# Optimization experiments

Measured on AMD Instinct MI355X. Metric: run time of the kernel, lower is better.

The kernel has to match this reference:

```python
import jax, jax.numpy as jnp
import numpy as np

N_NODES = 100000


def gcn_conv(x, W, b, src, dst, num_nodes):
    # PyG GCNConv: add self-loops, symmetric normalization, x @ W, scatter-add, + b
    xw = x @ W  # [N, out]
    loop = jnp.arange(num_nodes, dtype=src.dtype)
    s = jnp.concatenate([src, loop])  # message source j
    d = jnp.concatenate([dst, loop])  # aggregation target i
    deg = jax.ops.segment_sum(jnp.ones_like(d, dtype=xw.dtype), d, num_segments=num_nodes)
    dis = jnp.where(deg > 0, jax.lax.rsqrt(deg), 0.0)  # D^{-1/2}
    norm = dis[s] * dis[d]  # [E+N]
    msg = norm[:, None] * xw[s]  # gather + scale
    out = jax.ops.segment_sum(msg, d, num_segments=num_nodes)  # scatter-add
    return out + b


def setup_inputs() -> dict:
    key = jax.random.key(0)
    k1, k2, k3, k4 = jax.random.split(key, 4)
    F, H, E = 64, 64, 1250000
    x = jax.random.normal(k1, (N_NODES, F), dtype=jnp.float32)
    edge_index = jax.random.randint(k2, (2, E), 0, N_NODES, dtype=jnp.int64)
    W1 = jax.random.normal(k3, (F, H), dtype=jnp.float32) * (1.0 / np.sqrt(F))
    b1 = jnp.zeros((H,), dtype=jnp.float32)
    W2 = jax.random.normal(k4, (H, F), dtype=jnp.float32) * (1.0 / np.sqrt(H))
    b2 = jnp.zeros((F,), dtype=jnp.float32)
    return {"x": x, "edge_index": edge_index, "W1": W1, "b1": b1, "W2": W2, "b2": b2}


def reference(x, edge_index, W1, b1, W2, b2):
    src, dst = edge_index[0], edge_index[1]
    h = gcn_conv(x, W1, b1, src, dst, N_NODES)
    h = jax.nn.relu(h)
    out = gcn_conv(h, W2, b2, src, dst, N_NODES)
    return out
```

## Files before the change

kernel.cpp:

```cpp
#include <hip/hip_runtime.h>

#define NN    100000
#define F     64
#define NBUCK 391
#define CAPB  4096
#define TILE  4096
#define G1A   1600
#define G1TOT 3125

#define O_CURSOR 0
#define O_ROWPTR 512
#define O_DEG    100864
#define O_DIS    201216
#define O_PACKED 301568
#define O_SRT    1903104
#define O_AH     3504768
#define O_BH     6704768

__device__ __forceinline__ unsigned bf_rne(float x) {
    unsigned u = __float_as_uint(x);
    return (u + 0x7FFFu + ((u >> 16) & 1u)) >> 16;
}
__device__ __forceinline__ unsigned pack2(float lo, float hi) {
    return bf_rne(lo) | (bf_rne(hi) << 16);
}
__device__ __forceinline__ float lo_f(unsigned u) { return __uint_as_float(u << 16); }
__device__ __forceinline__ float hi_f(unsigned u) { return __uint_as_float(u & 0xFFFF0000u); }

struct BpSmem {
    int hist[NBUCK], lofs[NBUCK], gbase[NBUCK], lcur[NBUCK];
    int wsum[8];
    unsigned stage[TILE];
    unsigned short sbuck[TILE];
};
union KSmem {
    BpSmem bp;
    float wl[64 * 64];
};
struct NsSmem {
    int h[256], lcur[256], wsum[4];
    int stage[CAPB];
};
union K2Smem {
    NsSmem ns;
    float wl[64 * 64];
};

__device__ __forceinline__ void binpack_body(const int* __restrict__ src,
                                             const int* __restrict__ dst, int E,
                                             int* __restrict__ cursor,
                                             unsigned* __restrict__ packed,
                                             int bid, BpSmem& sm) {
    int t  = threadIdx.x;
    int t0 = bid * TILE;
    int n  = min(TILE, E - t0);

    if (t < NBUCK) sm.hist[t] = 0;
    __syncthreads();
    for (int i = t; i < n; i += 512) atomicAdd(&sm.hist[dst[t0 + i] >> 8], 1);
    __syncthreads();
    int lane = t & 63, w = t >> 6;
    int v = (t < NBUCK) ? sm.hist[t] : 0;
    int s = v;
#pragma unroll
    for (int off = 1; off < 64; off <<= 1) {
        int u = __shfl_up(s, off, 64);
        if (lane >= off) s += u;
    }
    if (lane == 63) sm.wsum[w] = s;
    __syncthreads();
    if (t == 0) {
        int run = 0;
#pragma unroll
        for (int i = 0; i < 8; ++i) { int c = sm.wsum[i]; sm.wsum[i] = run; run += c; }
    }
    __syncthreads();
    if (t < NBUCK) {
        int ex = s - v + sm.wsum[w];
        sm.lofs[t] = ex;
        sm.lcur[t] = ex;
        sm.gbase[t] = t * CAPB + (v ? atomicAdd(&cursor[t], v) : 0);
    }
    __syncthreads();
    for (int i = t; i < n; i += 512) {
        int d = dst[t0 + i];
        int b = d >> 8;
        int p = atomicAdd(&sm.lcur[b], 1);
        sm.stage[p] = ((unsigned)src[t0 + i] << 8) | (unsigned)(d & 255);
        sm.sbuck[p] = (unsigned short)b;
    }
    __syncthreads();
    for (int i = t; i < n; i += 512) {
        int b = sm.sbuck[i];
        packed[sm.gbase[b] + (i - sm.lofs[b])] = sm.stage[i];
    }
}

__device__ __forceinline__ void gemm_body(const float* __restrict__ X,
                                          const float* __restrict__ W,
                                          unsigned* __restrict__ Ah, int bid,
                                          float* wl) {
    int t = threadIdx.x;
    for (int i = t; i < 64 * 64; i += 512) wl[i] = W[i];
    __syncthreads();
    int lane = t & 63;
    int w    = t >> 6;
    float Wreg[64];
#pragma unroll
    for (int k = 0; k < 64; ++k) Wreg[k] = wl[k * 64 + lane];

    int row0 = bid * 32 + w * 4;
    const float* xp = X + (size_t)row0 * F;
    float xa = xp[lane];
    float xb = xp[64 + lane];
    float xc = xp[128 + lane];
    float xd = xp[192 + lane];
    float a0 = 0.f, a1 = 0.f, a2 = 0.f, a3 = 0.f;
#pragma unroll
    for (int k = 0; k < 64; ++k) {
        float wv = Wreg[k];
        a0 = fmaf(__uint_as_float(__builtin_amdgcn_readlane(__float_as_uint(xa), k)), wv, a0);
        a1 = fmaf(__uint_as_float(__builtin_amdgcn_readlane(__float_as_uint(xb), k)), wv, a1);
        a2 = fmaf(__uint_as_float(__builtin_amdgcn_readlane(__float_as_uint(xc), k)), wv, a2);
        a3 = fmaf(__uint_as_float(__builtin_amdgcn_readlane(__float_as_uint(xd), k)), wv, a3);
    }
    float p0 = __shfl_xor(a0, 1, 64);
    float p1 = __shfl_xor(a1, 1, 64);
    float p2 = __shfl_xor(a2, 1, 64);
    float p3 = __shfl_xor(a3, 1, 64);
    if (!(lane & 1)) {
        int c = lane >> 1;
        Ah[(size_t)(row0 + 0) * 32 + c] = pack2(a0, p0);
        Ah[(size_t)(row0 + 1) * 32 + c] = pack2(a1, p1);
        Ah[(size_t)(row0 + 2) * 32 + c] = pack2(a2, p2);
        Ah[(size_t)(row0 + 3) * 32 + c] = pack2(a3, p3);
    }
}

__device__ __forceinline__ void node_sort_body(const unsigned* __restrict__ packed,
                                               const int* __restrict__ cursor,
                                               int* __restrict__ row_ptr,
                                               int* __restrict__ deg,
                                               float* __restrict__ dis,
                                               int* __restrict__ srt,
                                               int b, NsSmem& sm) {
    int t = threadIdx.x;
    int nbase = b << 8;
    int nloc = min(256, NN - nbase);
    int beg = b * CAPB;
    int n = cursor[b];

    if (t < 256) sm.h[t] = 0;
    __syncthreads();
    for (int i = t; i < n; i += 512)
        atomicAdd(&sm.h[packed[beg + i] & 255u], 1);
    __syncthreads();
    int lane = t & 63, w = t >> 6;
    int v = 0, s = 0;
    if (t < 256) { v = sm.h[t]; s = v; }
#pragma unroll
    for (int off = 1; off < 64; off <<= 1) {
        int u = __shfl_up(s, off, 64);
        if (lane >= off) s += u;
    }
    if (t < 256 && lane == 63) sm.wsum[w] = s;
    __syncthreads();
    if (t == 0) {
        int run = 0;
#pragma unroll
        for (int i = 0; i < 4; ++i) { int c = sm.wsum[i]; sm.wsum[i] = run; run += c; }
    }
    __syncthreads();
    if (t < 256) {
        int e0 = s - v + sm.wsum[w];
        sm.lcur[t] = e0;
        if (t < nloc) {
            row_ptr[nbase + t] = beg + e0;
            deg[nbase + t]     = v;
            dis[nbase + t]     = rsqrtf((float)v + 1.0f);
        }
    }
    __syncthreads();
    for (int i = t; i < n; i += 512) {
        unsigned p = packed[beg + i];
        int pos = atomicAdd(&sm.lcur[p & 255u], 1);
        sm.stage[pos] = (int)(p >> 8);
    }
    __syncthreads();
    for (int i = t; i < n; i += 512) srt[beg + i] = sm.stage[i];
}

__global__ __launch_bounds__(512) void pre_gemm1(const int* __restrict__ src,
                                                 const int* __restrict__ dst, int E,
                                                 int nbp, int* __restrict__ cursor,
                                                 unsigned* __restrict__ packed,
                                                 const float* __restrict__ X,
                                                 const float* __restrict__ W1,
                                                 unsigned* __restrict__ Ah) {
    __shared__ KSmem sm;
    if ((int)blockIdx.x < nbp)
        binpack_body(src, dst, E, cursor, packed, blockIdx.x, sm.bp);
    else
        gemm_body(X, W1, Ah, (int)blockIdx.x - nbp, sm.wl);
}

__global__ __launch_bounds__(512) void sort_gemm1(const unsigned* __restrict__ packed,
                                                  const int* __restrict__ cursor,
                                                  int* __restrict__ row_ptr,
                                                  int* __restrict__ deg,
                                                  float* __restrict__ dis,
                                                  int* __restrict__ srt,
                                                  const float* __restrict__ X,
                                                  const float* __restrict__ W1,
                                                  unsigned* __restrict__ Ah) {
    __shared__ K2Smem sm;
    if ((int)blockIdx.x < NBUCK)
        node_sort_body(packed, cursor, row_ptr, deg, dis, srt, blockIdx.x, sm.ns);
    else
        gemm_body(X, W1, Ah, G1A + (int)blockIdx.x - NBUCK, sm.wl);
}

__global__ __launch_bounds__(256) void agg1_gemm2(const uint2* __restrict__ Ah2,
                                                  const int* __restrict__ row_ptr,
                                                  const int* __restrict__ deg,
                                                  const int* __restrict__ srt,
                                                  const float* __restrict__ dis,
                                                  const float* __restrict__ b1,
                                                  const float* __restrict__ W2,
                                                  unsigned* __restrict__ Bh) {
    __shared__ float wl[64 * 64];
    int t = threadIdx.x;
    for (int i = t; i < 64 * 64; i += 256) wl[i] = W2[i];
    __syncthreads();

    int sub  = t & 15;
    int node = blockIdx.x * 16 + (t >> 4);
    int beg = row_ptr[node];
    int end = beg + deg[node];
    float di = dis[node];
    uint2 su = Ah2[(size_t)node * 16 + sub];
    float4 acc;
    acc.x = di * lo_f(su.x);
    acc.y = di * hi_f(su.x);
    acc.z = di * lo_f(su.y);
    acc.w = di * hi_f(su.y);
    int j = beg;
    for (; j + 4 <= end; j += 4) {
        int s0 = srt[j], s1 = srt[j + 1], s2 = srt[j + 2], s3 = srt[j + 3];
        float d0 = dis[s0], d1 = dis[s1], d2 = dis[s2], d3 = dis[s3];
        uint2 g0 = Ah2[(size_t)s0 * 16 + sub];
        uint2 g1 = Ah2[(size_t)s1 * 16 + sub];
        uint2 g2 = Ah2[(size_t)s2 * 16 + sub];
        uint2 g3 = Ah2[(size_t)s3 * 16 + sub];
        acc.x = fmaf(d0, lo_f(g0.x), fmaf(d1, lo_f(g1.x), fmaf(d2, lo_f(g2.x), fmaf(d3, lo_f(g3.x), acc.x))));
        acc.y = fmaf(d0, hi_f(g0.x), fmaf(d1, hi_f(g1.x), fmaf(d2, hi_f(g2.x), fmaf(d3, hi_f(g3.x), acc.y))));
        acc.z = fmaf(d0, lo_f(g0.y), fmaf(d1, lo_f(g1.y), fmaf(d2, lo_f(g2.y), fmaf(d3, lo_f(g3.y), acc.z))));
        acc.w = fmaf(d0, hi_f(g0.y), fmaf(d1, hi_f(g1.y), fmaf(d2, hi_f(g2.y), fmaf(d3, hi_f(g3.y), acc.w))));
    }
    for (; j < end; ++j) {
        int s0 = srt[j];
        float d0 = dis[s0];
        uint2 g0 = Ah2[(size_t)s0 * 16 + sub];
        acc.x = fmaf(d0, lo_f(g0.x), acc.x);
        acc.y = fmaf(d0, hi_f(g0.x), acc.y);
        acc.z = fmaf(d0, lo_f(g0.y), acc.z);
        acc.w = fmaf(d0, hi_f(g0.y), acc.w);
    }
    float4 bb = ((const float4*)b1)[sub];
    float4 o;
    o.x = fmaxf(fmaf(di, acc.x, bb.x), 0.f);
    o.y = fmaxf(fmaf(di, acc.y, bb.y), 0.f);
    o.z = fmaxf(fmaf(di, acc.z, bb.z), 0.f);
    o.w = fmaxf(fmaf(di, acc.w, bb.w), 0.f);
    unsigned pkx = pack2(o.x, o.y);
    unsigned pky = pack2(o.z, o.w);

    int lane = t & 63;
    float a0 = 0.f, a1 = 0.f, a2 = 0.f, a3 = 0.f;
#pragma unroll
    for (int kq = 0; kq < 16; ++kq) {
        float w0 = wl[(4 * kq + 0) * 64 + lane];
        float w1 = wl[(4 * kq + 1) * 64 + lane];
        float w2 = wl[(4 * kq + 2) * 64 + lane];
        float w3 = wl[(4 * kq + 3) * 64 + lane];
        unsigned qx0 = __builtin_amdgcn_readlane(pkx, kq);
        unsigned qy0 = __builtin_amdgcn_readlane(pky, kq);
        unsigned qx1 = __builtin_amdgcn_readlane(pkx, 16 + kq);
        unsigned qy1 = __builtin_amdgcn_readlane(pky, 16 + kq);
        unsigned qx2 = __builtin_amdgcn_readlane(pkx, 32 + kq);
        unsigned qy2 = __builtin_amdgcn_readlane(pky, 32 + kq);
        unsigned qx3 = __builtin_amdgcn_readlane(pkx, 48 + kq);
        unsigned qy3 = __builtin_amdgcn_readlane(pky, 48 + kq);
        a0 = fmaf(lo_f(qx0), w0, a0); a0 = fmaf(hi_f(qx0), w1, a0);
        a0 = fmaf(lo_f(qy0), w2, a0); a0 = fmaf(hi_f(qy0), w3, a0);
        a1 = fmaf(lo_f(qx1), w0, a1); a1 = fmaf(hi_f(qx1), w1, a1);
        a1 = fmaf(lo_f(qy1), w2, a1); a1 = fmaf(hi_f(qy1), w3, a1);
        a2 = fmaf(lo_f(qx2), w0, a2); a2 = fmaf(hi_f(qx2), w1, a2);
        a2 = fmaf(lo_f(qy2), w2, a2); a2 = fmaf(hi_f(qy2), w3, a2);
        a3 = fmaf(lo_f(qx3), w0, a3); a3 = fmaf(hi_f(qx3), w1, a3);
        a3 = fmaf(lo_f(qy3), w2, a3); a3 = fmaf(hi_f(qy3), w3, a3);
    }
    float p0 = __shfl_xor(a0, 1, 64);
    float p1 = __shfl_xor(a1, 1, 64);
    float p2 = __shfl_xor(a2, 1, 64);
    float p3 = __shfl_xor(a3, 1, 64);
    if (!(lane & 1)) {
        int c = lane >> 1;
        int row0 = blockIdx.x * 16 + (t >> 6) * 4;
        Bh[(size_t)(row0 + 0) * 32 + c] = pack2(a0, p0);
        Bh[(size_t)(row0 + 1) * 32 + c] = pack2(a1, p1);
        Bh[(size_t)(row0 + 2) * 32 + c] = pack2(a2, p2);
        Bh[(size_t)(row0 + 3) * 32 + c] = pack2(a3, p3);
    }
}

__global__ __launch_bounds__(256) void agg_out(const uint2* __restrict__ Ah2,
                                               const int* __restrict__ row_ptr,
                                               const int* __restrict__ deg,
                                               const int* __restrict__ srt,
                                               const float* __restrict__ dis,
                                               const float* __restrict__ bias,
                                               float* __restrict__ outp) {
    int sub  = threadIdx.x & 15;
    int node = blockIdx.x * 16 + (threadIdx.x >> 4);
    int beg = row_ptr[node];
    int end = beg + deg[node];
    float di = dis[node];
    uint2 su = Ah2[(size_t)node * 16 + sub];
    float4 acc;
    acc.x = di * lo_f(su.x);
    acc.y = di * hi_f(su.x);
    acc.z = di * lo_f(su.y);
    acc.w = di * hi_f(su.y);
    int j = beg;
    for (; j + 4 <= end; j += 4) {
        int s0 = srt[j], s1 = srt[j + 1], s2 = srt[j + 2], s3 = srt[j + 3];
        float d0 = dis[s0], d1 = dis[s1], d2 = dis[s2], d3 = dis[s3];
        uint2 g0 = Ah2[(size_t)s0 * 16 + sub];
        uint2 g1 = Ah2[(size_t)s1 * 16 + sub];
        uint2 g2 = Ah2[(size_t)s2 * 16 + sub];
        uint2 g3 = Ah2[(size_t)s3 * 16 + sub];
        acc.x = fmaf(d0, lo_f(g0.x), fmaf(d1, lo_f(g1.x), fmaf(d2, lo_f(g2.x), fmaf(d3, lo_f(g3.x), acc.x))));
        acc.y = fmaf(d0, hi_f(g0.x), fmaf(d1, hi_f(g1.x), fmaf(d2, hi_f(g2.x), fmaf(d3, hi_f(g3.x), acc.y))));
        acc.z = fmaf(d0, lo_f(g0.y), fmaf(d1, lo_f(g1.y), fmaf(d2, lo_f(g2.y), fmaf(d3, lo_f(g3.y), acc.z))));
        acc.w = fmaf(d0, hi_f(g0.y), fmaf(d1, hi_f(g1.y), fmaf(d2, hi_f(g2.y), fmaf(d3, hi_f(g3.y), acc.w))));
    }
    for (; j < end; ++j) {
        int s0 = srt[j];
        float d0 = dis[s0];
        uint2 g0 = Ah2[(size_t)s0 * 16 + sub];
        acc.x = fmaf(d0, lo_f(g0.x), acc.x);
        acc.y = fmaf(d0, hi_f(g0.x), acc.y);
        acc.z = fmaf(d0, lo_f(g0.y), acc.z);
        acc.w = fmaf(d0, hi_f(g0.y), acc.w);
    }
    float4 bb = ((const float4*)bias)[sub];
    float4 o;
    o.x = fmaf(di, acc.x, bb.x);
    o.y = fmaf(di, acc.y, bb.y);
    o.z = fmaf(di, acc.z, bb.z);
    o.w = fmaf(di, acc.w, bb.w);
    ((float4*)outp)[(size_t)node * 16 + sub] = o;
}

extern "C" void kernel_launch(void* const* d_in, const int* in_sizes, int n_in,
                              void* d_out, int out_size, void* d_ws, size_t ws_size,
                              hipStream_t stream) {
    const float* x  = (const float*)d_in[0];
    const int*   ei = (const int*)d_in[1];
    const float* W1 = (const float*)d_in[2];
    const float* b1 = (const float*)d_in[3];
    const float* W2 = (const float*)d_in[4];
    const float* b2 = (const float*)d_in[5];
    float* out = (float*)d_out;
    int E = in_sizes[1] / 2;
    const int* src = ei;
    const int* dst = ei + E;

    int*      ws_i    = (int*)d_ws;
    int*      cursor  = ws_i + O_CURSOR;
    int*      row_ptr = ws_i + O_ROWPTR;
    int*      deg     = ws_i + O_DEG;
    float*    dis     = (float*)(ws_i + O_DIS);
    unsigned* packed  = (unsigned*)(ws_i + O_PACKED);
    int*      srt     = ws_i + O_SRT;
    unsigned* Ah      = (unsigned*)(ws_i + O_AH);
    unsigned* Bh      = (unsigned*)(ws_i + O_BH);

    int nbp = (E + TILE - 1) / TILE;

    hipMemsetAsync(cursor, 0, NBUCK * sizeof(int), stream);
    pre_gemm1<<<nbp + G1A, 512, 0, stream>>>(src, dst, E, nbp, cursor, packed,
                                             x, W1, Ah);
    sort_gemm1<<<NBUCK + (G1TOT - G1A), 512, 0, stream>>>(packed, cursor, row_ptr,
                                                          deg, dis, srt, x, W1, Ah);
    agg1_gemm2<<<NN / 16, 256, 0, stream>>>((const uint2*)Ah, row_ptr, deg, srt,
                                            dis, b1, W2, Bh);
    agg_out<<<NN / 16, 256, 0, stream>>>((const uint2*)Bh, row_ptr, deg, srt,
                                         dis, b2, out);
}
```

Baseline: 200.7 us.

## Use 16-byte gathers with two-way edge split and prescale layer-2 output by dis

The two aggregation kernels now have each lane gather a uint4 (8 bf16 features) instead of a uint2. The 16 threads per node are split into two groups that take alternating edges and combine their partial sums with a cross-lane shuffle. The layer-2 GEMM output is premultiplied by the source node's dis, so the final aggregation drops the per-edge dis lookup and multiply. This aims to cut memory transactions and per-edge dependent loads, but adds a reduction shuffle and uses more registers per thread.

```diff
diff --git a/kernel.cpp b/kernel.cpp
--- a/kernel.cpp
+++ b/kernel.cpp
@@ -220,7 +220,7 @@
         gemm_body(X, W1, Ah, G1A + (int)blockIdx.x - NBUCK, sm.wl);
 }
 
-__global__ __launch_bounds__(256) void agg1_gemm2(const uint2* __restrict__ Ah2,
+__global__ __launch_bounds__(256) void agg1_gemm2(const uint4* __restrict__ Ah4,
                                                   const int* __restrict__ row_ptr,
                                                   const int* __restrict__ deg,
                                                   const int* __restrict__ srt,
@@ -230,137 +230,219 @@
                                                   unsigned* __restrict__ Bh) {
     __shared__ float wl[64 * 64];
     int t = threadIdx.x;
-    for (int i = t; i < 64 * 64; i += 256) wl[i] = W2[i];
-    __syncthreads();
-
-    int sub  = t & 15;
+    for (int i = t; i < 1024; i += 256)
+        ((float4*)wl)[i] = ((const float4*)W2)[i];
+    __syncthreads();
+
+    int sub  = t & 7;
+    int grp  = (t >> 3) & 1;
     int node = blockIdx.x * 16 + (t >> 4);
     int beg = row_ptr[node];
     int end = beg + deg[node];
     float di = dis[node];
-    uint2 su = Ah2[(size_t)node * 16 + sub];
-    float4 acc;
-    acc.x = di * lo_f(su.x);
-    acc.y = di * hi_f(su.x);
-    acc.z = di * lo_f(su.y);
-    acc.w = di * hi_f(su.y);
-    int j = beg;
-    for (; j + 4 <= end; j += 4) {
-        int s0 = srt[j], s1 = srt[j + 1], s2 = srt[j + 2], s3 = srt[j + 3];
+
+    float a0, a1, a2, a3, a4, a5, a6, a7;
+    uint4 su = Ah4[(size_t)node * 8 + sub];
+    if (grp == 0) {
+        a0 = di * lo_f(su.x); a1 = di * hi_f(su.x);
+        a2 = di * lo_f(su.y); a3 = di * hi_f(su.y);
+        a4 = di * lo_f(su.z); a5 = di * hi_f(su.z);
+        a6 = di * lo_f(su.w); a7 = di * hi_f(su.w);
+    } else {
+        a0 = a1 = a2 = a3 = a4 = a5 = a6 = a7 = 0.f;
+    }
+
+    int j = beg + grp;
+    for (; j + 6 < end; j += 8) {
+        int s0 = srt[j], s1 = srt[j + 2], s2 = srt[j + 4], s3 = srt[j + 6];
         float d0 = dis[s0], d1 = dis[s1], d2 = dis[s2], d3 = dis[s3];
-        uint2 g0 = Ah2[(size_t)s0 * 16 + sub];
-        uint2 g1 = Ah2[(size_t)s1 * 16 + sub];
-        uint2 g2 = Ah2[(size_t)s2 * 16 + sub];
-        uint2 g3 = Ah2[(size_t)s3 * 16 + sub];
-        acc.x = fmaf(d0, lo_f(g0.x), fmaf(d1, lo_f(g1.x), fmaf(d2, lo_f(g2.x), fmaf(d3, lo_f(g3.x), acc.x))));
-        acc.y = fmaf(d0, hi_f(g0.x), fmaf(d1, hi_f(g1.x), fmaf(d2, hi_f(g2.x), fmaf(d3, hi_f(g3.x), acc.y))));
-        acc.z = fmaf(d0, lo_f(g0.y), fmaf(d1, lo_f(g1.y), fmaf(d2, lo_f(g2.y), fmaf(d3, lo_f(g3.y), acc.z))));
-        acc.w = fmaf(d0, hi_f(g0.y), fmaf(d1, hi_f(g1.y), fmaf(d2, hi_f(g2.y), fmaf(d3, hi_f(g3.y), acc.w))));
-    }
-    for (; j < end; ++j) {
+        uint4 g0 = Ah4[(size_t)s0 * 8 + sub];
+        uint4 g1 = Ah4[(size_t)s1 * 8 + sub];
+        uint4 g2 = Ah4[(size_t)s2 * 8 + sub];
+        uint4 g3 = Ah4[(size_t)s3 * 8 + sub];
+        a0 = fmaf(d0, lo_f(g0.x), fmaf(d1, lo_f(g1.x), fmaf(d2, lo_f(g2.x), fmaf(d3, lo_f(g3.x), a0))));
+        a1 = fmaf(d0, hi_f(g0.x), fmaf(d1, hi_f(g1.x), fmaf(d2, hi_f(g2.x), fmaf(d3, hi_f(g3.x), a1))));
+        a2 = fmaf(d0, lo_f(g0.y), fmaf(d1, lo_f(g1.y), fmaf(d2, lo_f(g2.y), fmaf(d3, lo_f(g3.y), a2))));
+        a3 = fmaf(d0, hi_f(g0.y), fmaf(d1, hi_f(g1.y), fmaf(d2, hi_f(g2.y), fmaf(d3, hi_f(g3.y), a3))));
+        a4 = fmaf(d0, lo_f(g0.z), fmaf(d1, lo_f(g1.z), fmaf(d2, lo_f(g2.z), fmaf(d3, lo_f(g3.z), a4))));
+        a5 = fmaf(d0, hi_f(g0.z), fmaf(d1, hi_f(g1.z), fmaf(d2, hi_f(g2.z), fmaf(d3, hi_f(g3.z), a5))));
+        a6 = fmaf(d0, lo_f(g0.w), fmaf(d1, lo_f(g1.w), fmaf(d2, lo_f(g2.w), fmaf(d3, lo_f(g3.w), a6))));
+        a7 = fmaf(d0, hi_f(g0.w), fmaf(d1, hi_f(g1.w), fmaf(d2, hi_f(g2.w), fmaf(d3, hi_f(g3.w), a7))));
+    }
+    for (; j + 2 < end; j += 4) {
+        int s0 = srt[j], s1 = srt[j + 2];
+        float d0 = dis[s0], d1 = dis[s1];
+        uint4 g0 = Ah4[(size_t)s0 * 8 + sub];
+        uint4 g1 = Ah4[(size_t)s1 * 8 + sub];
+        a0 = fmaf(d0, lo_f(g0.x), fmaf(d1, lo_f(g1.x), a0));
+        a1 = fmaf(d0, hi_f(g0.x), fmaf(d1, hi_f(g1.x), a1));
+        a2 = fmaf(d0, lo_f(g0.y), fmaf(d1, lo_f(g1.y), a2));
+        a3 = fmaf(d0, hi_f(g0.y), fmaf(d1, hi_f(g1.y), a3));
+        a4 = fmaf(d0, lo_f(g0.z), fmaf(d1, lo_f(g1.z), a4));
+        a5 = fmaf(d0, hi_f(g0.z), fmaf(d1, hi_f(g1.z), a5));
+        a6 = fmaf(d0, lo_f(g0.w), fmaf(d1, lo_f(g1.w), a6));
+        a7 = fmaf(d0, hi_f(g0.w), fmaf(d1, hi_f(g1.w), a7));
+    }
+    for (; j < end; j += 2) {
         int s0 = srt[j];
         float d0 = dis[s0];
-        uint2 g0 = Ah2[(size_t)s0 * 16 + sub];
-        acc.x = fmaf(d0, lo_f(g0.x), acc.x);
-        acc.y = fmaf(d0, hi_f(g0.x), acc.y);
-        acc.z = fmaf(d0, lo_f(g0.y), acc.z);
-        acc.w = fmaf(d0, hi_f(g0.y), acc.w);
-    }
-    float4 bb = ((const float4*)b1)[sub];
-    float4 o;
-    o.x = fmaxf(fmaf(di, acc.x, bb.x), 0.f);
-    o.y = fmaxf(fmaf(di, acc.y, bb.y), 0.f);
-    o.z = fmaxf(fmaf(di, acc.z, bb.z), 0.f);
-    o.w = fmaxf(fmaf(di, acc.w, bb.w), 0.f);
-    unsigned pkx = pack2(o.x, o.y);
-    unsigned pky = pack2(o.z, o.w);
+        uint4 g0 = Ah4[(size_t)s0 * 8 + sub];
+        a0 = fmaf(d0, lo_f(g0.x), a0);
+        a1 = fmaf(d0, hi_f(g0.x), a1);
+        a2 = fmaf(d0, lo_f(g0.y), a2);
+        a3 = fmaf(d0, hi_f(g0.y), a3);
+        a4 = fmaf(d0, lo_f(g0.z), a4);
+        a5 = fmaf(d0, hi_f(g0.z), a5);
+        a6 = fmaf(d0, lo_f(g0.w), a6);
+        a7 = fmaf(d0, hi_f(g0.w), a7);
+    }
+    a0 += __shfl_xor(a0, 8, 64); a1 += __shfl_xor(a1, 8, 64);
+    a2 += __shfl_xor(a2, 8, 64); a3 += __shfl_xor(a3, 8, 64);
+    a4 += __shfl_xor(a4, 8, 64); a5 += __shfl_xor(a5, 8, 64);
+    a6 += __shfl_xor(a6, 8, 64); a7 += __shfl_xor(a7, 8, 64);
+
+    float4 bb0 = ((const float4*)b1)[2 * sub];
+    float4 bb1 = ((const float4*)b1)[2 * sub + 1];
+    float o0 = fmaxf(fmaf(di, a0, bb0.x), 0.f);
+    float o1 = fmaxf(fmaf(di, a1, bb0.y), 0.f);
+    float o2 = fmaxf(fmaf(di, a2, bb0.z), 0.f);
+    float o3 = fmaxf(fmaf(di, a3, bb0.w), 0.f);
+    float o4 = fmaxf(fmaf(di, a4, bb1.x), 0.f);
+    float o5 = fmaxf(fmaf(di, a5, bb1.y), 0.f);
+    float o6 = fmaxf(fmaf(di, a6, bb1.z), 0.f);
+    float o7 = fmaxf(fmaf(di, a7, bb1.w), 0.f);
+    unsigned pk0 = pack2(o0, o1);
+    unsigned pk1 = pack2(o2, o3);
+    unsigned pk2 = pack2(o4, o5);
+    unsigned pk3 = pack2(o6, o7);
 
     int lane = t & 63;
-    float a0 = 0.f, a1 = 0.f, a2 = 0.f, a3 = 0.f;
-#pragma unroll
-    for (int kq = 0; kq < 16; ++kq) {
-        float w0 = wl[(4 * kq + 0) * 64 + lane];
-        float w1 = wl[(4 * kq + 1) * 64 + lane];
-        float w2 = wl[(4 * kq + 2) * 64 + lane];
-        float w3 = wl[(4 * kq + 3) * 64 + lane];
-        unsigned qx0 = __builtin_amdgcn_readlane(pkx, kq);
-        unsigned qy0 = __builtin_amdgcn_readlane(pky, kq);
-        unsigned qx1 = __builtin_amdgcn_readlane(pkx, 16 + kq);
-        unsigned qy1 = __builtin_amdgcn_readlane(pky, 16 + kq);
-        unsigned qx2 = __builtin_amdgcn_readlane(pkx, 32 + kq);
-        unsigned qy2 = __builtin_amdgcn_readlane(pky, 32 + kq);
-        unsigned qx3 = __builtin_amdgcn_readlane(pkx, 48 + kq);
-        unsigned qy3 = __builtin_amdgcn_readlane(pky, 48 + kq);
-        a0 = fmaf(lo_f(qx0), w0, a0); a0 = fmaf(hi_f(qx0), w1, a0);
-        a0 = fmaf(lo_f(qy0), w2, a0); a0 = fmaf(hi_f(qy0), w3, a0);
-        a1 = fmaf(lo_f(qx1), w0, a1); a1 = fmaf(hi_f(qx1), w1, a1);
-        a1 = fmaf(lo_f(qy1), w2, a1); a1 = fmaf(hi_f(qy1), w3, a1);
-        a2 = fmaf(lo_f(qx2), w0, a2); a2 = fmaf(hi_f(qx2), w1, a2);
-        a2 = fmaf(lo_f(qy2), w2, a2); a2 = fmaf(hi_f(qy2), w3, a2);
-        a3 = fmaf(lo_f(qx3), w0, a3); a3 = fmaf(hi_f(qx3), w1, a3);
-        a3 = fmaf(lo_f(qy3), w2, a3); a3 = fmaf(hi_f(qy3), w3, a3);
-    }
-    float p0 = __shfl_xor(a0, 1, 64);
-    float p1 = __shfl_xor(a1, 1, 64);
-    float p2 = __shfl_xor(a2, 1, 64);
-    float p3 = __shfl_xor(a3, 1, 64);
+    float c0 = 0.f, c1 = 0.f, c2 = 0.f, c3 = 0.f;
+#pragma unroll
+    for (int l8 = 0; l8 < 8; ++l8) {
+#define STEP(PK, P)                                                        \
+        {                                                                  \
+            int k0 = l8 * 8 + 2 * (P);                                     \
+            float w0 = wl[k0 * 64 + lane];                                 \
+            float w1 = wl[k0 * 64 + 64 + lane];                            \
+            unsigned u0 = __builtin_amdgcn_readlane(PK, l8);               \
+            unsigned u1 = __builtin_amdgcn_readlane(PK, 16 + l8);          \
+            unsigned u2 = __builtin_amdgcn_readlane(PK, 32 + l8);          \
+            unsigned u3 = __builtin_amdgcn_readlane(PK, 48 + l8);          \
+            c0 = fmaf(lo_f(u0), w0, c0); c0 = fmaf(hi_f(u0), w1, c0);      \
+            c1 = fmaf(lo_f(u1), w0, c1); c1 = fmaf(hi_f(u1), w1, c1);      \
+            c2 = fmaf(lo_f(u2), w0, c2); c2 = fmaf(hi_f(u2), w1, c2);      \
+            c3 = fmaf(lo_f(u3), w0, c3); c3 = fmaf(hi_f(u3), w1, c3);      \
+        }
+        STEP(pk0, 0)
+        STEP(pk1, 1)
+        STEP(pk2, 2)
+        STEP(pk3, 3)
+#undef STEP
+    }
+    float dA = __shfl(di, 0, 64);
+    float dB = __shfl(di, 16, 64);
+    float dC = __shfl(di, 32, 64);
+    float dD = __shfl(di, 48, 64);
+    c0 *= dA; c1 *= dB; c2 *= dC; c3 *= dD;
+    float q0 = __shfl_xor(c0, 1, 64);
+    float q1 = __shfl_xor(c1, 1, 64);
+    float q2 = __shfl_xor(c2, 1, 64);
+    float q3 = __shfl_xor(c3, 1, 64);
     if (!(lane & 1)) {
         int c = lane >> 1;
-        int row0 = blockIdx.x * 16 + (t >> 6) * 4;
-        Bh[(size_t)(row0 + 0) * 32 + c] = pack2(a0, p0);
-        Bh[(size_t)(row0 + 1) * 32 + c] = pack2(a1, p1);
-        Bh[(size_t)(row0 + 2) * 32 + c] = pack2(a2, p2);
-        Bh[(size_t)(row0 + 3) * 32 + c] = pack2(a3, p3);
-    }
-}
-
-__global__ __launch_bounds__(256) void agg_out(const uint2* __restrict__ Ah2,
+        int n0 = blockIdx.x * 16 + (t >> 6) * 4;
+        Bh[(size_t)(n0 + 0) * 32 + c] = pack2(c0, q0);
+        Bh[(size_t)(n0 + 1) * 32 + c] = pack2(c1, q1);
+        Bh[(size_t)(n0 + 2) * 32 + c] = pack2(c2, q2);
+        Bh[(size_t)(n0 + 3) * 32 + c] = pack2(c3, q3);
+    }
+}
+
+__global__ __launch_bounds__(256) void agg_out(const uint4* __restrict__ Bs4,
                                                const int* __restrict__ row_ptr,
                                                const int* __restrict__ deg,
                                                const int* __restrict__ srt,
                                                const float* __restrict__ dis,
                                                const float* __restrict__ bias,
                                                float* __restrict__ outp) {
-    int sub  = threadIdx.x & 15;
-    int node = blockIdx.x * 16 + (threadIdx.x >> 4);
+    int t = threadIdx.x;
+    int sub  = t & 7;
+    int grp  = (t >> 3) & 1;
+    int node = blockIdx.x * 16 + (t >> 4);
     int beg = row_ptr[node];
     int end = beg + deg[node];
     float di = dis[node];
-    uint2 su = Ah2[(size_t)node * 16 + sub];
-    float4 acc;
-    acc.x = di * lo_f(su.x);
-    acc.y = di * hi_f(su.x);
-    acc.z = di * lo_f(su.y);
-    acc.w = di * hi_f(su.y);
-    int j = beg;
-    for (; j + 4 <= end; j += 4) {
-        int s0 = srt[j], s1 = srt[j + 1], s2 = srt[j + 2], s3 = srt[j + 3];
-        float d0 = dis[s0], d1 = dis[s1], d2 = dis[s2], d3 = dis[s3];
-        uint2 g0 = Ah2[(size_t)s0 * 16 + sub];
-        uint2 g1 = Ah2[(size_t)s1 * 16 + sub];
-        uint2 g2 = Ah2[(size_t)s2 * 16 + sub];
-        uint2 g3 = Ah2[(size_t)s3 * 16 + sub];
-        acc.x = fmaf(d0, lo_f(g0.x), fmaf(d1, lo_f(g1.x), fmaf(d2, lo_f(g2.x), fmaf(d3, lo_f(g3.x), acc.x))));
-        acc.y = fmaf(d0, hi_f(g0.x), fmaf(d1, hi_f(g1.x), fmaf(d2, hi_f(g2.x), fmaf(d3, hi_f(g3.x), acc.y))));
-        acc.z = fmaf(d0, lo_f(g0.y), fmaf(d1, lo_f(g1.y), fmaf(d2, lo_f(g2.y), fmaf(d3, lo_f(g3.y), acc.z))));
-        acc.w = fmaf(d0, hi_f(g0.y), fmaf(d1, hi_f(g1.y), fmaf(d2, hi_f(g2.y), fmaf(d3, hi_f(g3.y), acc.w))));
-    }
-    for (; j < end; ++j) {
+
+    float a0, a1, a2, a3, a4, a5, a6, a7;
+    uint4 su = Bs4[(size_t)node * 8 + sub];
+    if (grp == 0) {
+        a0 = lo_f(su.x); a1 = hi_f(su.x);
+        a2 = lo_f(su.y); a3 = hi_f(su.y);
+        a4 = lo_f(su.z); a5 = hi_f(su.z);
+        a6 = lo_f(su.w); a7 = hi_f(su.w);
+    } else {
+        a0 = a1 = a2 = a3 = a4 = a5 = a6 = a7 = 0.f;
+    }
+
+    int j = beg + grp;
+    for (; j + 6 < end; j += 8) {
+        int s0 = srt[j], s1 = srt[j + 2], s2 = srt[j + 4], s3 = srt[j + 6];
+        uint4 g0 = Bs4[(size_t)s0 * 8 + sub];
+        uint4 g1 = Bs4[(size_t)s1 * 8 + sub];
+        uint4 g2 = Bs4[(size_t)s2 * 8 + sub];
+        uint4 g3 = Bs4[(size_t)s3 * 8 + sub];
+        a0 += (lo_f(g0.x) + lo_f(g1.x)) + (lo_f(g2.x) + lo_f(g3.x));
+        a1 += (hi_f(g0.x) + hi_f(g1.x)) + (hi_f(g2.x) + hi_f(g3.x));
+        a2 += (lo_f(g0.y) + lo_f(g1.y)) + (lo_f(g2.y) + lo_f(g3.y));
+        a3 += (hi_f(g0.y) + hi_f(g1.y)) + (hi_f(g2.y) + hi_f(g3.y));
+        a4 += (lo_f(g0.z) + lo_f(g1.z)) + (lo_f(g2.z) + lo_f(g3.z));
+        a5 += (hi_f(g0.z) + hi_f(g1.z)) + (hi_f(g2.z) + hi_f(g3.z));
+        a6 += (lo_f(g0.w) + lo_f(g1.w)) + (lo_f(g2.w) + lo_f(g3.w));
+        a7 += (hi_f(g0.w) + hi_f(g1.w)) + (hi_f(g2.w) + hi_f(g3.w));
+    }
+    for (; j + 2 < end; j += 4) {
+        int s0 = srt[j], s1 = srt[j + 2];
+        uint4 g0 = Bs4[(size_t)s0 * 8 + sub];
+        uint4 g1 = Bs4[(size_t)s1 * 8 + sub];
+        a0 += lo_f(g0.x) + lo_f(g1.x);
+        a1 += hi_f(g0.x) + hi_f(g1.x);
+        a2 += lo_f(g0.y) + lo_f(g1.y);
+        a3 += hi_f(g0.y) + hi_f(g1.y);
+        a4 += lo_f(g0.z) + lo_f(g1.z);
+        a5 += hi_f(g0.z) + hi_f(g1.z);
+        a6 += lo_f(g0.w) + lo_f(g1.w);
+        a7 += hi_f(g0.w) + hi_f(g1.w);
+    }
+    for (; j < end; j += 2) {
         int s0 = srt[j];
-        float d0 = dis[s0];
-        uint2 g0 = Ah2[(size_t)s0 * 16 + sub];
-        acc.x = fmaf(d0, lo_f(g0.x), acc.x);
-        acc.y = fmaf(d0, hi_f(g0.x), acc.y);
-        acc.z = fmaf(d0, lo_f(g0.y), acc.z);
-        acc.w = fmaf(d0, hi_f(g0.y), acc.w);
-    }
-    float4 bb = ((const float4*)bias)[sub];
+        uint4 g0 = Bs4[(size_t)s0 * 8 + sub];
+        a0 += lo_f(g0.x); a1 += hi_f(g0.x);
+        a2 += lo_f(g0.y); a3 += hi_f(g0.y);
+        a4 += lo_f(g0.z); a5 += hi_f(g0.z);
+        a6 += lo_f(g0.w); a7 += hi_f(g0.w);
+    }
+    a0 += __shfl_xor(a0, 8, 64); a1 += __shfl_xor(a1, 8, 64);
+    a2 += __shfl_xor(a2, 8, 64); a3 += __shfl_xor(a3, 8, 64);
+    a4 += __shfl_xor(a4, 8, 64); a5 += __shfl_xor(a5, 8, 64);
+    a6 += __shfl_xor(a6, 8, 64); a7 += __shfl_xor(a7, 8, 64);
+
+    float4 bb0 = ((const float4*)bias)[2 * sub];
+    float4 bb1 = ((const float4*)bias)[2 * sub + 1];
     float4 o;
-    o.x = fmaf(di, acc.x, bb.x);
-    o.y = fmaf(di, acc.y, bb.y);
-    o.z = fmaf(di, acc.z, bb.z);
-    o.w = fmaf(di, acc.w, bb.w);
-    ((float4*)outp)[(size_t)node * 16 + sub] = o;
+    if (grp == 0) {
+        o.x = fmaf(di, a0, bb0.x);
+        o.y = fmaf(di, a1, bb0.y);
+        o.z = fmaf(di, a2, bb0.z);
+        o.w = fmaf(di, a3, bb0.w);
+        ((float4*)outp)[(size_t)node * 16 + 2 * sub] = o;
+    } else {
+        o.x = fmaf(di, a4, bb1.x);
+        o.y = fmaf(di, a5, bb1.y);
+        o.z = fmaf(di, a6, bb1.z);
+        o.w = fmaf(di, a7, bb1.w);
+        ((float4*)outp)[(size_t)node * 16 + 2 * sub + 1] = o;
+    }
 }
 
 extern "C" void kernel_launch(void* const* d_in, const int* in_sizes, int n_in,
@@ -394,8 +476,8 @@
                                              x, W1, Ah);
     sort_gemm1<<<NBUCK + (G1TOT - G1A), 512, 0, stream>>>(packed, cursor, row_ptr,
                                                           deg, dis, srt, x, W1, Ah);
-    agg1_gemm2<<<NN / 16, 256, 0, stream>>>((const uint2*)Ah, row_ptr, deg, srt,
+    agg1_gemm2<<<NN / 16, 256, 0, stream>>>((const uint4*)Ah, row_ptr, deg, srt,
                                             dis, b1, W2, Bh);
-    agg_out<<<NN / 16, 256, 0, stream>>>((const uint2*)Bh, row_ptr, deg, srt,
+    agg_out<<<NN / 16, 256, 0, stream>>>((const uint4*)Bh, row_ptr, deg, srt,
                                          dis, b2, out);
 }
```

Result: faster. 193.1 us (-3.8%).
